# Kernel tuning notes

Measured on AMD Instinct MI355X. Metric: run time of the kernel, lower is better.

## Reference

```python
import jax, jax.numpy as jnp
import numpy as np

B, S, D = 2, 2048, 768
E, F = 8, 3072  # num_experts, d_ff


def setup_inputs() -> dict:
    key = jax.random.key(0)
    k1, k2, k3, k4 = jax.random.split(key, 4)
    hidden_states = jax.random.normal(k1, (B, S, D), dtype=jnp.float32)
    w_router = jax.random.normal(k2, (D, E), dtype=jnp.float32) * (D ** -0.5)
    w1 = jax.random.normal(k3, (E, D, F), dtype=jnp.float32) * (D ** -0.5)
    w2 = jax.random.normal(k4, (E, F, D), dtype=jnp.float32) * (F ** -0.5)
    return {"hidden_states": hidden_states, "w_router": w_router, "w1": w1, "w2": w2}


def reference(hidden_states, w_router, w1, w2):
    # Router: top-1 (switch) routing.
    router_logits = jnp.einsum("bsd,de->bse", hidden_states, w_router)
    probs = jax.nn.softmax(router_logits, axis=-1)
    expert_index = jnp.argmax(probs, axis=-1)                      # [B,S] int
    router_mask = jax.nn.one_hot(expert_index, E, dtype=hidden_states.dtype)  # [B,S,E]
    router_probs = jnp.max(probs, axis=-1, keepdims=True)          # [B,S,1]

    # Expert FFN dispatch/combine (world_size=1 -> all_to_all is identity):
    # each token is processed by its assigned expert's relu-MLP.
    h1 = jax.nn.relu(jnp.einsum("bsd,edf->ebsf", hidden_states, w1))  # [E,B,S,F]
    h2 = jnp.einsum("ebsf,efd->ebsd", h1, w2)                          # [E,B,S,D]
    expert_out = jnp.einsum("ebsd,bse->bsd", h2, router_mask)          # combine

    out = router_probs * expert_out
    return out, router_logits, expert_index
```

## Files before the change

### kernel.cpp

```cpp
#include <hip/hip_runtime.h>
#include <hip/hip_bf16.h>

#define B_ 2
#define S_ 2048
#define D_ 768
#define E_ 8
#define F_ 3072
#define NT (B_*S_)

typedef __attribute__((ext_vector_type(8))) short bf16x8;
typedef __attribute__((ext_vector_type(4))) float f32x4;
typedef __attribute__((ext_vector_type(8))) unsigned short u16x8;

__device__ __forceinline__ unsigned short f2bf(float f){
  __hip_bfloat16 h = __float2bfloat16(f);
  return *reinterpret_cast<unsigned short*>(&h);
}

__device__ __forceinline__ void gll16(const void* g, void* l){
  __builtin_amdgcn_global_load_lds((const __attribute__((address_space(1))) unsigned int*)g,
                                   (__attribute__((address_space(3))) unsigned int*)l,
                                   16, 0, 0);
}

__global__ __launch_bounds__(256) void router_kernel(
    const float* __restrict__ x, const float* __restrict__ wr,
    float* __restrict__ logits_out, float* __restrict__ idx_out,
    float* __restrict__ probs, int* __restrict__ counts,
    int* __restrict__ bucket, unsigned short* __restrict__ xbf)
{
  const int wave = threadIdx.x >> 6, lane = threadIdx.x & 63;
  const int token = blockIdx.x * 4 + wave;
  const float* xp = x + (size_t)token * D_;

  float acc[E_] = {0.f,0.f,0.f,0.f,0.f,0.f,0.f,0.f};
  float xv[12];
  #pragma unroll
  for (int i = 0; i < 12; ++i){
    const int d = lane + i*64;
    const float v = xp[d];
    xv[i] = v;
    const float4 w0 = *(const float4*)(wr + d*8);
    const float4 w1 = *(const float4*)(wr + d*8 + 4);
    acc[0] += v*w0.x; acc[1] += v*w0.y; acc[2] += v*w0.z; acc[3] += v*w0.w;
    acc[4] += v*w1.x; acc[5] += v*w1.y; acc[6] += v*w1.z; acc[7] += v*w1.w;
  }
  #pragma unroll
  for (int j = 0; j < E_; ++j){
    float a = acc[j];
    for (int off = 32; off > 0; off >>= 1) a += __shfl_xor(a, off);
    acc[j] = a;
  }
  #pragma unroll
  for (int i = 0; i < 12; ++i){
    const int d = lane + i*64;
    xbf[(size_t)token * D_ + d] = f2bf(xv[i]);
  }
  if (lane == 0){
    float m = acc[0];
    #pragma unroll
    for (int j = 1; j < E_; ++j) m = fmaxf(m, acc[j]);
    float p[E_]; float s = 0.f;
    #pragma unroll
    for (int j = 0; j < E_; ++j){ p[j] = expf(acc[j] - m); s += p[j]; }
    const float inv = 1.0f / s;
    int best = 0; float bp = p[0]*inv;
    #pragma unroll
    for (int j = 1; j < E_; ++j){ const float pj = p[j]*inv; if (pj > bp){ bp = pj; best = j; } }
    float* lo = logits_out + (size_t)token * E_;
    #pragma unroll
    for (int j = 0; j < E_; ++j) lo[j] = acc[j];
    idx_out[token] = (float)best;
    probs[token] = bp;
    const int pos = atomicAdd(&counts[best], 1);
    bucket[best * NT + pos] = token;
  }
}

__global__ __launch_bounds__(256) void transpose_cvt(
    const float* __restrict__ in, unsigned short* __restrict__ outp, int R, int C)
{
  __shared__ float tile[64][65];
  const int e = blockIdx.z;
  const int r0 = blockIdx.y << 6, c0 = blockIdx.x << 6;
  const float* src = in + (size_t)e * R * C;
  unsigned short* dst = outp + (size_t)e * R * C;
  const int tid = threadIdx.x;
  {
    const int lr = tid >> 4, lc = (tid & 15) << 2;
    #pragma unroll
    for (int rr = 0; rr < 4; ++rr){
      const int row = (rr << 4) + lr;
      const float4 v = *(const float4*)(src + (size_t)(r0 + row) * C + c0 + lc);
      tile[row][lc+0] = v.x; tile[row][lc+1] = v.y;
      tile[row][lc+2] = v.z; tile[row][lc+3] = v.w;
    }
  }
  __syncthreads();
  {
    const int wr = tid >> 3, wc = (tid & 7) << 3;
    #pragma unroll
    for (int it = 0; it < 2; ++it){
      const int crow = (it << 5) + wr;
      u16x8 o;
      #pragma unroll
      for (int j = 0; j < 8; ++j) o[j] = f2bf(tile[wc + j][crow]);
      *(u16x8*)(dst + (size_t)(c0 + crow) * R + r0 + wc) = o;
    }
  }
}

template<int K, int NCOLS, bool RELU>
__global__ __launch_bounds__(256) void gemm_grouped(
    const unsigned short* __restrict__ Ab, const unsigned short* __restrict__ Bt,
    const int* __restrict__ counts, const int* __restrict__ bucket,
    const float* __restrict__ probs, unsigned short* __restrict__ h1out,
    float* __restrict__ fout)
{
  __shared__ unsigned short As[64*64];
  __shared__ unsigned short Bs[128*64];
  const int e = blockIdx.z, mt = blockIdx.y, nt = blockIdx.x;
  const int cnt = counts[e];
  if ((mt << 6) >= cnt) return;
  const int fbase = nt << 7;
  const int tid = threadIdx.x, wave = tid >> 6, lane = tid & 63;
  const int* bkt = bucket + e * NT;

  const int inrow = (lane & 7) << 4;
  const int rsub  = lane >> 3;
  const int rowA0 = (wave << 4) + rsub;
  const int rowA1 = rowA0 + 8;
  const int cm1 = cnt - 1;
  int gA0 = (mt << 6) + rowA0; if (gA0 > cm1) gA0 = cm1;
  int gA1 = (mt << 6) + rowA1; if (gA1 > cm1) gA1 = cm1;
  const int t0 = bkt[gA0], t1 = bkt[gA1];
  const char* pA0 = (const char*)Ab + (size_t)t0 * (K*2) + (inrow ^ ((rowA0 & 7) << 4));
  const char* pA1 = (const char*)Ab + (size_t)t1 * (K*2) + (inrow ^ ((rowA1 & 7) << 4));
  char* lA0 = (char*)As + (wave << 11);
  char* lA1 = lA0 + 1024;

  const char* pB[4];
  char* lB[4];
  #pragma unroll
  for (int c = 0; c < 4; ++c){
    const int rowB = (wave << 5) + (c << 3) + rsub;
    pB[c] = (const char*)Bt + (size_t)(e * NCOLS + fbase + rowB) * (K*2)
            + (inrow ^ ((rowB & 7) << 4));
    lB[c] = (char*)Bs + (wave << 12) + (c << 10);
  }

  f32x4 acc[4][2] = {};
  const char* AsB = (const char*)As;
  const char* BsB = (const char*)Bs;
  const int lo16 = lane & 15;
  const int hi = lane >> 4;

  for (int kt = 0; kt < K/64; ++kt){
    const int off = kt << 7;
    gll16(pA0 + off, lA0);
    gll16(pA1 + off, lA1);
    gll16(pB[0] + off, lB[0]);
    gll16(pB[1] + off, lB[1]);
    gll16(pB[2] + off, lB[2]);
    gll16(pB[3] + off, lB[3]);
    __syncthreads();
    #pragma unroll
    for (int kf = 0; kf < 2; ++kf){
      const int ko = (kf << 6) + (hi << 4);
      bf16x8 af[4], bfr[2];
      #pragma unroll
      for (int mf = 0; mf < 4; ++mf){
        const int row = (mf << 4) + lo16;
        af[mf] = *(const bf16x8*)(AsB + row*128 + (ko ^ ((row & 7) << 4)));
      }
      #pragma unroll
      for (int nf = 0; nf < 2; ++nf){
        const int col = (wave << 5) + (nf << 4) + lo16;
        bfr[nf] = *(const bf16x8*)(BsB + col*128 + (ko ^ ((col & 7) << 4)));
      }
      #pragma unroll
      for (int mf = 0; mf < 4; ++mf)
        #pragma unroll
        for (int nf = 0; nf < 2; ++nf)
          acc[mf][nf] = __builtin_amdgcn_mfma_f32_16x16x32_bf16(af[mf], bfr[nf], acc[mf][nf], 0, 0, 0);
    }
    __syncthreads();
  }

  const int rem = cnt - (mt << 6);
  #pragma unroll
  for (int mf = 0; mf < 4; ++mf){
    #pragma unroll
    for (int j = 0; j < 4; ++j){
      const int r = (mf << 4) + (hi << 2) + j;
      if (r < rem){
        const int tok = bkt[(mt << 6) + r];
        if constexpr (RELU){
          #pragma unroll
          for (int nf = 0; nf < 2; ++nf){
            float v = acc[mf][nf][j];
            v = v > 0.f ? v : 0.f;
            h1out[(size_t)tok * NCOLS + fbase + (wave << 5) + (nf << 4) + lo16] = f2bf(v);
          }
        } else {
          const float p = probs[tok];
          #pragma unroll
          for (int nf = 0; nf < 2; ++nf)
            fout[(size_t)tok * NCOLS + fbase + (wave << 5) + (nf << 4) + lo16] = p * acc[mf][nf][j];
        }
      }
    }
  }
}

extern "C" void kernel_launch(void* const* d_in, const int* in_sizes, int n_in,
                              void* d_out, int out_size, void* d_ws, size_t ws_size,
                              hipStream_t stream)
{
  const float* x  = (const float*)d_in[0];
  const float* wr = (const float*)d_in[1];
  const float* w1 = (const float*)d_in[2];
  const float* w2 = (const float*)d_in[3];
  float* out = (float*)d_out;

  constexpr size_t OUT_L = (size_t)NT * D_;
  constexpr size_t OUT_I = OUT_L + (size_t)NT * E_;

  char* ws = (char*)d_ws;
  int*            counts = (int*)ws;
  float*          probs  = (float*)(ws + 1024);
  int*            bucket = (int*)(ws + (32u << 10));
  unsigned short* xbf    = (unsigned short*)(ws + (256u << 10));
  unsigned short* w1t    = (unsigned short*)(ws + (8ull  << 20));
  unsigned short* w2t    = (unsigned short*)(ws + (48ull << 20));
  unsigned short* h1     = (unsigned short*)(ws + (88ull << 20));

  hipMemsetAsync(counts, 0, E_ * sizeof(int), stream);

  router_kernel<<<dim3(NT/4), dim3(256), 0, stream>>>(
      x, wr, out + OUT_L, out + OUT_I, probs, counts, bucket, xbf);

  transpose_cvt<<<dim3(F_/64, D_/64, E_), dim3(256), 0, stream>>>(w1, w1t, D_, F_);
  transpose_cvt<<<dim3(D_/64, F_/64, E_), dim3(256), 0, stream>>>(w2, w2t, F_, D_);

  gemm_grouped<D_, F_, true><<<dim3(F_/128, 64, E_), dim3(256), 0, stream>>>(
      xbf, w1t, counts, bucket, nullptr, h1, nullptr);

  gemm_grouped<F_, D_, false><<<dim3(D_/128, 64, E_), dim3(256), 0, stream>>>(
      h1, w2t, counts, bucket, probs, nullptr, out);
}
```

Baseline: 349.8 us.

## Use 128x128 double-buffered grouped GEMM with compact tile list and contiguous h1

Replaces the 64-row grouped GEMM with a 128x128 tile per block, where each wave computes a 64x64 quadrant, and double-buffers LDS so the next K-slice loads while the current one is computed. A small kernel builds a compact list of (expert, m-tile) pairs, so the grid no longer launches mostly-empty blocks across the E x 64 space. The intermediate h1 is now stored contiguously per expert, so the second GEMM reads its A rows without gathering through the bucket. The larger tile doubles the accumulator registers and the LDS footprint, which may lower occupancy, and MAXTILES=40 relies on per-expert tile counts summing to at most 40.

```diff
diff --git a/kernel.cpp b/kernel.cpp
--- a/kernel.cpp
+++ b/kernel.cpp
@@ -7,6 +7,8 @@
 #define E_ 8
 #define F_ 3072
 #define NT (B_*S_)
+#define BM 128
+#define MAXTILES 40
 
 typedef __attribute__((ext_vector_type(8))) short bf16x8;
 typedef __attribute__((ext_vector_type(4))) float f32x4;
@@ -77,6 +79,21 @@
   }
 }
 
+__global__ void build_tiles(const int* __restrict__ counts, int* __restrict__ meta)
+{
+  if (threadIdx.x == 0 && blockIdx.x == 0){
+    int off = 0, n = 0;
+    for (int e = 0; e < E_; ++e){
+      const int c = counts[e];
+      meta[1+e] = off;
+      const int t = (c + BM - 1) / BM;
+      for (int m = 0; m < t; ++m){ meta[16 + n] = (e << 16) | m; ++n; }
+      off += c;
+    }
+    meta[0] = n;
+  }
+}
+
 __global__ __launch_bounds__(256) void transpose_cvt(
     const float* __restrict__ in, unsigned short* __restrict__ outp, int R, int C)
 {
@@ -98,115 +115,122 @@
   }
   __syncthreads();
   {
-    const int wr = tid >> 3, wc = (tid & 7) << 3;
+    const int wrr = tid >> 3, wcc = (tid & 7) << 3;
     #pragma unroll
     for (int it = 0; it < 2; ++it){
-      const int crow = (it << 5) + wr;
+      const int crow = (it << 5) + wrr;
       u16x8 o;
       #pragma unroll
-      for (int j = 0; j < 8; ++j) o[j] = f2bf(tile[wc + j][crow]);
-      *(u16x8*)(dst + (size_t)(c0 + crow) * R + r0 + wc) = o;
+      for (int j = 0; j < 8; ++j) o[j] = f2bf(tile[wcc + j][crow]);
+      *(u16x8*)(dst + (size_t)(c0 + crow) * R + r0 + wcc) = o;
     }
   }
 }
 
 template<int K, int NCOLS, bool RELU>
-__global__ __launch_bounds__(256) void gemm_grouped(
+__global__ __launch_bounds__(256) void gemm2ph(
     const unsigned short* __restrict__ Ab, const unsigned short* __restrict__ Bt,
     const int* __restrict__ counts, const int* __restrict__ bucket,
-    const float* __restrict__ probs, unsigned short* __restrict__ h1out,
-    float* __restrict__ fout)
-{
-  __shared__ unsigned short As[64*64];
-  __shared__ unsigned short Bs[128*64];
-  const int e = blockIdx.z, mt = blockIdx.y, nt = blockIdx.x;
-  const int cnt = counts[e];
-  if ((mt << 6) >= cnt) return;
-  const int fbase = nt << 7;
+    const int* __restrict__ meta, const float* __restrict__ probs,
+    unsigned short* __restrict__ h1out, float* __restrict__ fout)
+{
+  __shared__ unsigned short As[2][BM*64];
+  __shared__ unsigned short Bs[2][128*64];
+  if ((int)blockIdx.y >= meta[0]) return;
+  const int em = meta[16 + blockIdx.y];
+  const int e = em >> 16, mt = em & 0xffff;
+  const int cnt = counts[e], off_e = meta[1+e];
+  const int fbase = blockIdx.x << 7;
   const int tid = threadIdx.x, wave = tid >> 6, lane = tid & 63;
   const int* bkt = bucket + e * NT;
-
-  const int inrow = (lane & 7) << 4;
-  const int rsub  = lane >> 3;
-  const int rowA0 = (wave << 4) + rsub;
-  const int rowA1 = rowA0 + 8;
+  const int rbase = mt * BM;
+
+  const int rsub = lane >> 3;
+  const int swzb = ((lane & 7) ^ rsub) << 4;
   const int cm1 = cnt - 1;
-  int gA0 = (mt << 6) + rowA0; if (gA0 > cm1) gA0 = cm1;
-  int gA1 = (mt << 6) + rowA1; if (gA1 > cm1) gA1 = cm1;
-  const int t0 = bkt[gA0], t1 = bkt[gA1];
-  const char* pA0 = (const char*)Ab + (size_t)t0 * (K*2) + (inrow ^ ((rowA0 & 7) << 4));
-  const char* pA1 = (const char*)Ab + (size_t)t1 * (K*2) + (inrow ^ ((rowA1 & 7) << 4));
-  char* lA0 = (char*)As + (wave << 11);
-  char* lA1 = lA0 + 1024;
-
-  const char* pB[4];
-  char* lB[4];
+  const char* Asrc[4]; const char* Bsrc[4];
   #pragma unroll
   for (int c = 0; c < 4; ++c){
-    const int rowB = (wave << 5) + (c << 3) + rsub;
-    pB[c] = (const char*)Bt + (size_t)(e * NCOLS + fbase + rowB) * (K*2)
-            + (inrow ^ ((rowB & 7) << 4));
-    lB[c] = (char*)Bs + (wave << 12) + (c << 10);
-  }
-
-  f32x4 acc[4][2] = {};
-  const char* AsB = (const char*)As;
-  const char* BsB = (const char*)Bs;
-  const int lo16 = lane & 15;
-  const int hi = lane >> 4;
-
-  for (int kt = 0; kt < K/64; ++kt){
-    const int off = kt << 7;
-    gll16(pA0 + off, lA0);
-    gll16(pA1 + off, lA1);
-    gll16(pB[0] + off, lB[0]);
-    gll16(pB[1] + off, lB[1]);
-    gll16(pB[2] + off, lB[2]);
-    gll16(pB[3] + off, lB[3]);
-    __syncthreads();
+    const int cw = (c << 2) + wave;
+    const int row = (cw << 3) + rsub;
+    int gr = rbase + row; if (gr > cm1) gr = cm1;
+    const size_t arow = RELU ? (size_t)bkt[gr] : (size_t)(off_e + gr);
+    Asrc[c] = (const char*)(Ab + arow * K) + swzb;
+    Bsrc[c] = (const char*)(Bt + ((size_t)e * NCOLS + fbase + row) * K) + swzb;
+  }
+
+  f32x4 acc[4][4] = {};
+  const int wr = (wave >> 1) << 6;
+  const int wc = (wave & 1) << 6;
+  const int lo16 = lane & 15, hi = lane >> 4;
+  constexpr int KT = K / 64;
+
+  auto STAGE = [&](int buf, int kt){
+    const int kb = kt << 7;
+    #pragma unroll
+    for (int c = 0; c < 4; ++c){
+      const int cw = (c << 2) + wave;
+      gll16(Asrc[c] + kb, (char*)&As[buf][0] + (cw << 10));
+      gll16(Bsrc[c] + kb, (char*)&Bs[buf][0] + (cw << 10));
+    }
+  };
+  auto COMPUTE = [&](int buf){
+    const char* AsB = (const char*)&As[buf][0];
+    const char* BsB = (const char*)&Bs[buf][0];
     #pragma unroll
     for (int kf = 0; kf < 2; ++kf){
       const int ko = (kf << 6) + (hi << 4);
-      bf16x8 af[4], bfr[2];
+      bf16x8 af[4], bv[4];
       #pragma unroll
       for (int mf = 0; mf < 4; ++mf){
-        const int row = (mf << 4) + lo16;
-        af[mf] = *(const bf16x8*)(AsB + row*128 + (ko ^ ((row & 7) << 4)));
+        const int row = wr + (mf << 4) + lo16;
+        af[mf] = *(const bf16x8*)(AsB + row * 128 + (ko ^ ((row & 7) << 4)));
       }
       #pragma unroll
-      for (int nf = 0; nf < 2; ++nf){
-        const int col = (wave << 5) + (nf << 4) + lo16;
-        bfr[nf] = *(const bf16x8*)(BsB + col*128 + (ko ^ ((col & 7) << 4)));
+      for (int nf = 0; nf < 4; ++nf){
+        const int col = wc + (nf << 4) + lo16;
+        bv[nf] = *(const bf16x8*)(BsB + col * 128 + (ko ^ ((col & 7) << 4)));
       }
       #pragma unroll
       for (int mf = 0; mf < 4; ++mf)
         #pragma unroll
-        for (int nf = 0; nf < 2; ++nf)
-          acc[mf][nf] = __builtin_amdgcn_mfma_f32_16x16x32_bf16(af[mf], bfr[nf], acc[mf][nf], 0, 0, 0);
-    }
+        for (int nf = 0; nf < 4; ++nf)
+          acc[mf][nf] = __builtin_amdgcn_mfma_f32_16x16x32_bf16(af[mf], bv[nf], acc[mf][nf], 0, 0, 0);
+    }
+  };
+
+  STAGE(0, 0);
+  __syncthreads();
+  int cur = 0;
+  for (int kt = 0; kt < KT - 1; ++kt){
+    STAGE(cur ^ 1, kt + 1);
+    COMPUTE(cur);
     __syncthreads();
-  }
-
-  const int rem = cnt - (mt << 6);
+    cur ^= 1;
+  }
+  COMPUTE(cur);
+
+  const int rem = cnt - rbase;
   #pragma unroll
   for (int mf = 0; mf < 4; ++mf){
     #pragma unroll
     for (int j = 0; j < 4; ++j){
-      const int r = (mf << 4) + (hi << 2) + j;
+      const int r = wr + (mf << 4) + (hi << 2) + j;
       if (r < rem){
-        const int tok = bkt[(mt << 6) + r];
         if constexpr (RELU){
+          const size_t crow = (size_t)(off_e + rbase + r);
           #pragma unroll
-          for (int nf = 0; nf < 2; ++nf){
+          for (int nf = 0; nf < 4; ++nf){
             float v = acc[mf][nf][j];
             v = v > 0.f ? v : 0.f;
-            h1out[(size_t)tok * NCOLS + fbase + (wave << 5) + (nf << 4) + lo16] = f2bf(v);
+            h1out[crow * NCOLS + fbase + wc + (nf << 4) + lo16] = f2bf(v);
           }
         } else {
+          const int tok = bkt[rbase + r];
           const float p = probs[tok];
           #pragma unroll
-          for (int nf = 0; nf < 2; ++nf)
-            fout[(size_t)tok * NCOLS + fbase + (wave << 5) + (nf << 4) + lo16] = p * acc[mf][nf][j];
+          for (int nf = 0; nf < 4; ++nf)
+            fout[(size_t)tok * NCOLS + fbase + wc + (nf << 4) + lo16] = p * acc[mf][nf][j];
         }
       }
     }
@@ -228,24 +252,27 @@
 
   char* ws = (char*)d_ws;
   int*            counts = (int*)ws;
+  int*            meta   = (int*)(ws + 256);
   float*          probs  = (float*)(ws + 1024);
   int*            bucket = (int*)(ws + (32u << 10));
   unsigned short* xbf    = (unsigned short*)(ws + (256u << 10));
   unsigned short* w1t    = (unsigned short*)(ws + (8ull  << 20));
   unsigned short* w2t    = (unsigned short*)(ws + (48ull << 20));
-  unsigned short* h1     = (unsigned short*)(ws + (88ull << 20));
+  unsigned short* h1c    = (unsigned short*)(ws + (88ull << 20));
 
   hipMemsetAsync(counts, 0, E_ * sizeof(int), stream);
 
   router_kernel<<<dim3(NT/4), dim3(256), 0, stream>>>(
       x, wr, out + OUT_L, out + OUT_I, probs, counts, bucket, xbf);
 
+  build_tiles<<<dim3(1), dim3(64), 0, stream>>>(counts, meta);
+
   transpose_cvt<<<dim3(F_/64, D_/64, E_), dim3(256), 0, stream>>>(w1, w1t, D_, F_);
   transpose_cvt<<<dim3(D_/64, F_/64, E_), dim3(256), 0, stream>>>(w2, w2t, F_, D_);
 
-  gemm_grouped<D_, F_, true><<<dim3(F_/128, 64, E_), dim3(256), 0, stream>>>(
-      xbf, w1t, counts, bucket, nullptr, h1, nullptr);
-
-  gemm_grouped<F_, D_, false><<<dim3(D_/128, 64, E_), dim3(256), 0, stream>>>(
-      h1, w2t, counts, bucket, probs, nullptr, out);
-}
+  gemm2ph<D_, F_, true><<<dim3(F_/128, MAXTILES), dim3(256), 0, stream>>>(
+      xbf, w1t, counts, bucket, meta, nullptr, h1c, nullptr);
+
+  gemm2ph<F_, D_, false><<<dim3(D_/128, MAXTILES), dim3(256), 0, stream>>>(
+      h1c, w2t, counts, bucket, meta, probs, nullptr, out);
+}
```

Measured after the change: 339.8 us. -2.8%, faster.
